# Kernel tuning notes

Hardware: AMD Instinct MI355X
Metric: run time of the kernel (lower is better)

## Reference

```python
import jax, jax.numpy as jnp
import numpy as np
from jax import lax

B, CO, CI, KH, KW, H, W = 32, 128, 128, 3, 3, 56, 56
STRIDE = (1, 1)
PADDING = ((1, 1), (1, 1))


def setup_inputs() -> dict:
    key = jax.random.key(0)
    k1, k2, k3, k4 = jax.random.split(key, 4)
    inp = jax.random.normal(k1, (B, CI, H, W), dtype=jnp.float32)
    eps = jax.random.normal(k2, (B, CO, CI, KH, KW), dtype=jnp.float32)
    # reset_parameters: psi ~ U(-6, -5); mu ~ U(-stdv, stdv), stdv = 1/sqrt(CI*KH*KW)
    weight_psi = jax.random.uniform(k3, (CO, CI, KH, KW), dtype=jnp.float32,
                                    minval=-6.0, maxval=-5.0)
    stdv = 1.0 / np.sqrt(CI * KH * KW)
    weight_mu = jax.random.uniform(k4, (CO, CI, KH, KW), dtype=jnp.float32,
                                   minval=-stdv, maxval=stdv)
    return {"input": inp, "eps": eps, "weight_psi": weight_psi, "weight_mu": weight_mu}


def reference(input, eps, weight_psi, weight_mu):
    # mul_exp_add: per-sample weight = eps * exp(psi) + mu  -> [B, CO, CI, KH, KW]
    weight = eps * jnp.exp(weight_psi) + weight_mu

    # Per-example conv (torch does it via groups = bs trick); here vmap over batch.
    def conv_one(x, w):  # x: [CI,H,W], w: [CO,CI,KH,KW]
        return lax.conv_general_dilated(
            x[None], w, window_strides=STRIDE, padding=PADDING,
            dimension_numbers=("NCHW", "OIHW", "NCHW"))[0]

    out = jax.vmap(conv_one)(input, weight)  # [B, CO, H, W]
    return out
```

## Files before the change

### kernel.cpp

```cpp
#include <hip/hip_runtime.h>
#include <hip/hip_bf16.h>

#define CO    128
#define CI    128
#define NPIX  3136
#define PH    58
#define PPIX  3364
#define HPX   232
#define SROW  272

typedef __bf16 bf16x8 __attribute__((ext_vector_type(8)));
typedef float  f32x4  __attribute__((ext_vector_type(4)));

__global__ void prep_all(const float* __restrict__ in,
                         const float* __restrict__ eps,
                         const float* __restrict__ psi,
                         const float* __restrict__ mu,
                         __bf16* __restrict__ wt,
                         __bf16* __restrict__ it) {
  __shared__ __align__(16) char smem[32256];
  const int bx = blockIdx.x, tid = threadIdx.x;

  if (bx < 2048) {
    float* Ebuf = (float*)smem;
    float* Pbuf = (float*)(smem + 9216);
    float* Mbuf = (float*)(smem + 18432);
    __bf16* Wb  = (__bf16*)(smem + 27648);
    const int idx0  = bx * 256;
    const int b     = idx0 >> 14;
    const int coci0 = idx0 & 16383;
    const f32x4* esrc = (const f32x4*)(eps + (size_t)idx0 * 9);
    const f32x4* psrc = (const f32x4*)(psi + (size_t)coci0 * 9);
    const f32x4* msrc = (const f32x4*)(mu  + (size_t)coci0 * 9);
#pragma unroll
    for (int i = 0; i < 3; ++i) {
      int j = i * 256 + tid;
      if (j < 576) {
        ((f32x4*)Ebuf)[j] = esrc[j];
        ((f32x4*)Pbuf)[j] = psrc[j];
        ((f32x4*)Mbuf)[j] = msrc[j];
      }
    }
    __syncthreads();
#pragma unroll
    for (int p = 0; p < 9; ++p) {
      float v = Ebuf[tid * 9 + p] * __expf(Pbuf[tid * 9 + p]) + Mbuf[tid * 9 + p];
      Wb[p * 256 + tid] = (__bf16)v;
    }
    __syncthreads();
    __bf16* wb = wt + (size_t)b * 9 * CO * CI + coci0;
#pragma unroll
    for (int i = 0; i < 2; ++i) {
      int s = i * 256 + tid;
      if (s < 288) {
        int p = s >> 5, j = s & 31;
        *(f32x4*)(wb + (size_t)p * CO * CI + j * 8) =
            *(const f32x4*)&Wb[p * 256 + j * 8];
      }
    }
  } else if (bx < 2504) {
    int cid = (bx - 2048) * 256 + tid;
    int pid = cid >> 4;
    int chunk = cid & 15;
    int b = pid / 228;
    int e = pid - b * 228;
    int ph, pw;
    if (e < 58)       { ph = 0;       pw = e; }
    else if (e < 116) { ph = 57;      pw = e - 58; }
    else if (e < 172) { ph = e - 115; pw = 0; }
    else              { ph = e - 171; pw = 57; }
    f32x4 z = {0.f, 0.f, 0.f, 0.f};
    *(f32x4*)&it[((size_t)b * PPIX + ph * PH + pw) * CI + chunk * 8] = z;
  } else {
    __bf16 (*T)[136] = (__bf16(*)[136])smem;
    int tx = bx - 2504;
    int b  = tx / 49;
    int p0 = (tx - b * 49) * 64;
    const float* src = in + (size_t)b * CI * NPIX;
#pragma unroll
    for (int jj = 0; jj < 8; ++jj) {
      int c = jj * 256 + tid;
      int ci = c >> 4, xc = c & 15;
      float4 v = *(const float4*)(src + (size_t)ci * NPIX + p0 + xc * 4);
      T[xc * 4 + 0][ci] = (__bf16)v.x;
      T[xc * 4 + 1][ci] = (__bf16)v.y;
      T[xc * 4 + 2][ci] = (__bf16)v.z;
      T[xc * 4 + 3][ci] = (__bf16)v.w;
    }
    __syncthreads();
    __bf16* dstb = it + (size_t)b * PPIX * CI;
#pragma unroll
    for (int jj = 0; jj < 4; ++jj) {
      int c = jj * 256 + tid;
      int pl = c >> 4, xc = c & 15;
      int pix = p0 + pl;
      int oh = pix / 56, ow = pix - oh * 56;
      int ppix = (oh + 1) * PH + (ow + 1);
      *(f32x4*)&dstb[(size_t)ppix * CI + xc * 8] = *(const f32x4*)&T[pl][xc * 8];
    }
  }
}

__global__ __launch_bounds__(256) void bconv_gemm(
    const __bf16* __restrict__ wt,
    const __bf16* __restrict__ it,
    float* __restrict__ out) {
  __shared__ __align__(16) char Bsh[HPX * SROW];
  const int tid  = threadIdx.x;
  const int w    = tid >> 6;
  const int lane = tid & 63;
  const int quad = lane >> 4;
  const int l15  = lane & 15;

  const int lin = blockIdx.x;
  const int x   = lin & 7;
  const int j   = lin >> 3;
  const int bhi = j & 3;
  const int tile = j >> 2;
  const int b   = x + 8 * bhi;
  const int oh0 = tile * 2;

  const __bf16* hsrc = it + ((size_t)b * PPIX + oh0 * PH) * CI;
#pragma unroll
  for (int i = 0; i < 15; ++i) {
    int idx = i * 256 + tid;
    if (idx < HPX * 16) {
      int px = idx >> 4, sub = idx & 15;
      f32x4 v = *(const f32x4*)(hsrc + (size_t)idx * 8);
      *(f32x4*)&Bsh[px * SROW + sub * 16] = v;
    }
  }
  __syncthreads();

  int bbase[7];
#pragma unroll
  for (int nf = 0; nf < 7; ++nf) {
    int n = nf * 16 + l15;
    int r = (n >= 56) ? 1 : 0;
    int c = n - r * 56;
    bbase[nf] = (r * PH + c) * SROW + quad * 16;
  }

  const int co0 = w * 32;
  const __bf16* wtb = wt + (size_t)b * 9 * CO * CI;
  const int ab0 = (co0 +      l15) * CI + quad * 8;
  const int ab1 = (co0 + 16 + l15) * CI + quad * 8;

  f32x4 acc[2][7] = {};
  bf16x8 acur[2], anxt[2];
  acur[0] = *(const bf16x8*)(wtb + ab0);
  acur[1] = *(const bf16x8*)(wtb + ab1);

#pragma unroll
  for (int s = 0; s < 36; ++s) {
    const int p   = s >> 2;
    const int ci0 = (s & 3) << 5;
    if (s < 35) {
      const int pn   = (s + 1) >> 2;
      const int ci0n = ((s + 1) & 3) << 5;
      const __bf16* ap = wtb + pn * (CO * CI) + ci0n;
      anxt[0] = *(const bf16x8*)(ap + ab0);
      anxt[1] = *(const bf16x8*)(ap + ab1);
    }
    const int kh = p / 3, kw = p - kh * 3;
    const int tapb = (kh * PH + kw) * SROW + ci0 * 2;
#pragma unroll
    for (int nf = 0; nf < 7; ++nf) {
      bf16x8 bfr = *(const bf16x8*)&Bsh[bbase[nf] + tapb];
      acc[0][nf] = __builtin_amdgcn_mfma_f32_16x16x32_bf16(acur[0], bfr, acc[0][nf], 0, 0, 0);
      acc[1][nf] = __builtin_amdgcn_mfma_f32_16x16x32_bf16(acur[1], bfr, acc[1][nf], 0, 0, 0);
    }
    acur[0] = anxt[0];
    acur[1] = anxt[1];
  }

  float* ob = out + (size_t)b * CO * NPIX + oh0 * 56;
#pragma unroll
  for (int mf = 0; mf < 2; ++mf) {
#pragma unroll
    for (int nf = 0; nf < 7; ++nf) {
#pragma unroll
      for (int r = 0; r < 4; ++r) {
        int co = co0 + mf * 16 + quad * 4 + r;
        ob[(size_t)co * NPIX + nf * 16 + l15] = acc[mf][nf][r];
      }
    }
  }
}

extern "C" void kernel_launch(void* const* d_in, const int* in_sizes, int n_in,
                              void* d_out, int out_size, void* d_ws, size_t ws_size,
                              hipStream_t stream) {
  const float* inp = (const float*)d_in[0];
  const float* eps = (const float*)d_in[1];
  const float* psi = (const float*)d_in[2];
  const float* mu  = (const float*)d_in[3];

  __bf16* wt = (__bf16*)d_ws;
  __bf16* it = (__bf16*)((char*)d_ws + 9437184);

  prep_all<<<4072, 256, 0, stream>>>(inp, eps, psi, mu, wt, it);
  bconv_gemm<<<896, 256, 0, stream>>>(wt, it, (float*)d_out);
}
```

Baseline: 160.6 us.

## Split input channels into two halves to halve conv GEMM shared memory

The padded bf16 input is stored as two 64-channel planes per sample instead of one 128-channel plane. The GEMM kernel stages one half in shared memory, processes all 9 taps for it, then syncs and reloads the second half. This halves the LDS footprint (about 33KB instead of 63KB) and adds a launch-bounds hint of 4 blocks per SM, aiming for higher occupancy. The cost is a mid-loop barrier and a serialized reload of the second half, with no overlap against compute.

New measurement: 156.7 us. -2.4%, faster.

```diff
diff --git a/kernel.cpp b/kernel.cpp
--- a/kernel.cpp
+++ b/kernel.cpp
@@ -7,7 +7,7 @@
 #define PH    58
 #define PPIX  3364
 #define HPX   232
-#define SROW  272
+#define SROW2 144
 
 typedef __bf16 bf16x8 __attribute__((ext_vector_type(8)));
 typedef float  f32x4  __attribute__((ext_vector_type(4)));
@@ -62,6 +62,8 @@
     int cid = (bx - 2048) * 256 + tid;
     int pid = cid >> 4;
     int chunk = cid & 15;
+    int h  = chunk >> 3;
+    int c8 = chunk & 7;
     int b = pid / 228;
     int e = pid - b * 228;
     int ph, pw;
@@ -70,7 +72,7 @@
     else if (e < 172) { ph = e - 115; pw = 0; }
     else              { ph = e - 171; pw = 57; }
     f32x4 z = {0.f, 0.f, 0.f, 0.f};
-    *(f32x4*)&it[((size_t)b * PPIX + ph * PH + pw) * CI + chunk * 8] = z;
+    *(f32x4*)&it[((size_t)(b * 2 + h) * PPIX + ph * PH + pw) * 64 + c8 * 8] = z;
   } else {
     __bf16 (*T)[136] = (__bf16(*)[136])smem;
     int tx = bx - 2504;
@@ -88,24 +90,26 @@
       T[xc * 4 + 3][ci] = (__bf16)v.w;
     }
     __syncthreads();
-    __bf16* dstb = it + (size_t)b * PPIX * CI;
 #pragma unroll
     for (int jj = 0; jj < 4; ++jj) {
       int c = jj * 256 + tid;
       int pl = c >> 4, xc = c & 15;
+      int h  = xc >> 3;
+      int c8 = xc & 7;
       int pix = p0 + pl;
       int oh = pix / 56, ow = pix - oh * 56;
       int ppix = (oh + 1) * PH + (ow + 1);
-      *(f32x4*)&dstb[(size_t)ppix * CI + xc * 8] = *(const f32x4*)&T[pl][xc * 8];
+      *(f32x4*)&it[((size_t)(b * 2 + h) * PPIX + ppix) * 64 + c8 * 8] =
+          *(const f32x4*)&T[pl][xc * 8];
     }
   }
 }
 
-__global__ __launch_bounds__(256) void bconv_gemm(
+__global__ __launch_bounds__(256, 4) void bconv_gemm(
     const __bf16* __restrict__ wt,
     const __bf16* __restrict__ it,
     float* __restrict__ out) {
-  __shared__ __align__(16) char Bsh[HPX * SROW];
+  __shared__ __align__(16) char Bsh[HPX * SROW2];
   const int tid  = threadIdx.x;
   const int w    = tid >> 6;
   const int lane = tid & 63;
@@ -120,14 +124,14 @@
   const int b   = x + 8 * bhi;
   const int oh0 = tile * 2;
 
-  const __bf16* hsrc = it + ((size_t)b * PPIX + oh0 * PH) * CI;
-#pragma unroll
-  for (int i = 0; i < 15; ++i) {
+  const __bf16* hsrc0 = it + ((size_t)(b * 2 + 0) * PPIX + oh0 * PH) * 64;
+  const __bf16* hsrc1 = it + ((size_t)(b * 2 + 1) * PPIX + oh0 * PH) * 64;
+#pragma unroll
+  for (int i = 0; i < 8; ++i) {
     int idx = i * 256 + tid;
-    if (idx < HPX * 16) {
-      int px = idx >> 4, sub = idx & 15;
-      f32x4 v = *(const f32x4*)(hsrc + (size_t)idx * 8);
-      *(f32x4*)&Bsh[px * SROW + sub * 16] = v;
+    if (idx < HPX * 8) {
+      int px = idx >> 3, sub = idx & 7;
+      *(f32x4*)&Bsh[px * SROW2 + sub * 16] = *(const f32x4*)(hsrc0 + (size_t)idx * 8);
     }
   }
   __syncthreads();
@@ -138,7 +142,7 @@
     int n = nf * 16 + l15;
     int r = (n >= 56) ? 1 : 0;
     int c = n - r * 56;
-    bbase[nf] = (r * PH + c) * SROW + quad * 16;
+    bbase[nf] = (r * PH + c) * SROW2 + quad * 16;
   }
 
   const int co0 = w * 32;
@@ -153,17 +157,33 @@
 
 #pragma unroll
   for (int s = 0; s < 36; ++s) {
-    const int p   = s >> 2;
-    const int ci0 = (s & 3) << 5;
+    if (s == 18) {
+      __syncthreads();
+#pragma unroll
+      for (int i = 0; i < 8; ++i) {
+        int idx = i * 256 + tid;
+        if (idx < HPX * 8) {
+          int px = idx >> 3, sub = idx & 7;
+          *(f32x4*)&Bsh[px * SROW2 + sub * 16] = *(const f32x4*)(hsrc1 + (size_t)idx * 8);
+        }
+      }
+      __syncthreads();
+    }
+    const int s2 = s % 18;
+    const int p  = s2 >> 1;
+    const int kk = s2 & 1;
     if (s < 35) {
-      const int pn   = (s + 1) >> 2;
-      const int ci0n = ((s + 1) & 3) << 5;
-      const __bf16* ap = wtb + pn * (CO * CI) + ci0n;
+      const int sn  = s + 1;
+      const int hn  = sn / 18;
+      const int s2n = sn % 18;
+      const int pn  = s2n >> 1;
+      const int kkn = s2n & 1;
+      const __bf16* ap = wtb + pn * (CO * CI) + hn * 64 + kkn * 32;
       anxt[0] = *(const bf16x8*)(ap + ab0);
       anxt[1] = *(const bf16x8*)(ap + ab1);
     }
     const int kh = p / 3, kw = p - kh * 3;
-    const int tapb = (kh * PH + kw) * SROW + ci0 * 2;
+    const int tapb = (kh * PH + kw) * SROW2 + kk * 64;
 #pragma unroll
     for (int nf = 0; nf < 7; ++nf) {
       bf16x8 bfr = *(const bf16x8*)&Bsh[bbase[nf] + tapb];
```
